# Performance work log

Measured on AMD Instinct MI355X. Metric: run time of the kernel, lower is better.

Reference implementation:

```python
import jax, jax.numpy as jnp
import numpy as np

B, T, D, E, H = 4, 1024, 1024, 8, 2048


def setup_inputs() -> dict:
    key = jax.random.key(0)
    ks = jax.random.split(key, 5)
    # Kaiming-uniform-ish init scales (exact values irrelevant for correctness baseline)
    bound_bank = 1.0 / np.sqrt(D)
    bound_down = 1.0 / np.sqrt(H)
    return {
        "x": jax.random.normal(ks[0], (B, T, D), dtype=jnp.float32),
        "gate_w": jax.random.uniform(ks[1], (E, D), jnp.float32, -bound_bank, bound_bank),
        "gate_bank": jax.random.uniform(ks[2], (E, D, H), jnp.float32, -bound_bank, bound_bank),
        "up_bank": jax.random.uniform(ks[3], (E, D, H), jnp.float32, -bound_bank, bound_bank),
        "down_bank": jax.random.uniform(ks[4], (E, H, D), jnp.float32, -bound_down, bound_down),
    }


def reference(x, gate_w, gate_bank, up_bank, down_bank):
    # Router logits: [B,T,E] (nn.Linear with weight [E,D], no bias)
    logits = jnp.einsum('btd,ed->bte', x, gate_w)
    selected = jnp.argmax(logits, axis=-1)          # [B,T] int
    # Dense all-expert SwiGLU
    u = jnp.einsum('btd,edh->bteh', x, up_bank)     # [B,T,E,H]
    a = jnp.einsum('btd,edh->bteh', x, gate_bank)   # [B,T,E,H]
    h = jax.nn.silu(a) * u                          # [B,T,E,H]
    y = jnp.einsum('bteh,ehd->bted', h, down_bank)  # [B,T,E,D]
    # Gather argmax-selected expert output per token
    idx = selected[:, :, None, None]                # [B,T,1,1]
    out = jnp.take_along_axis(y, idx, axis=2)[:, :, 0, :]  # [B,T,D]
    return out
```

## Files before the change

kernel.cpp:

```cpp
#include <hip/hip_runtime.h>
#include <hip/hip_bf16.h>

#define NTOK 4096
#define DDIM 1024
#define HDIM 2048
#define NEXP 8

typedef __attribute__((ext_vector_type(4))) float f32x4;
typedef __attribute__((ext_vector_type(8))) short bf16x8;
typedef __attribute__((ext_vector_type(8))) unsigned short us8;

__device__ __forceinline__ unsigned short f2bf(float f) {
    unsigned u = __float_as_uint(f);
    return (unsigned short)((u + 0x7fffu + ((u >> 16) & 1u)) >> 16);
}

__device__ __forceinline__ void gload16(const void* g, void* l) {
    __builtin_amdgcn_global_load_lds((const __attribute__((address_space(1))) void*)g,
                                     (__attribute__((address_space(3))) void*)l, 16, 0, 0);
}

__global__ void xcast(const float* __restrict__ x, unsigned short* __restrict__ xb) {
    int i = blockIdx.x * blockDim.x + threadIdx.x;
    float4 v = reinterpret_cast<const float4*>(x)[i];
    ushort4 o = { f2bf(v.x), f2bf(v.y), f2bf(v.z), f2bf(v.w) };
    reinterpret_cast<ushort4*>(xb)[i] = o;
}

__global__ __launch_bounds__(256) void tcast(const float* __restrict__ src,
        unsigned short* __restrict__ dst, int R, int C, int interleave, int upoff,
        long long estride) {
    __shared__ unsigned short __attribute__((aligned(16))) tile[64][80];
    const int e = blockIdx.z, r0 = blockIdx.y * 64, c0 = blockIdx.x * 64;
    const float* s = src + ((size_t)e * R + r0) * C + c0;
    const int t = threadIdx.x;
    const int rd = t >> 2;
    #pragma unroll
    for (int j = 0; j < 4; ++j) {
        int c4 = (t & 3) * 4 + j;
        float4 v = *reinterpret_cast<const float4*>(s + (size_t)rd * C + c4 * 4);
        tile[c4 * 4 + 0][rd] = f2bf(v.x);
        tile[c4 * 4 + 1][rd] = f2bf(v.y);
        tile[c4 * 4 + 2][rd] = f2bf(v.z);
        tile[c4 * 4 + 3][rd] = f2bf(v.w);
    }
    __syncthreads();
    const int cr = t >> 2;
    const int c = c0 + cr;
    const int orow = interleave ? (((c >> 4) << 5) + (c & 15) + upoff) : c;
    unsigned short* drow = dst + (size_t)e * estride + (size_t)orow * R + r0;
    #pragma unroll
    for (int j = 0; j < 2; ++j) {
        int ch = (t & 3) + j * 4;
        *reinterpret_cast<us8*>(drow + ch * 8) = *reinterpret_cast<const us8*>(&tile[cr][ch * 8]);
    }
}

__global__ void gate_kernel(const float* __restrict__ x, const float* __restrict__ gw,
                            int* __restrict__ sel) {
    int t = blockIdx.x;
    int tid = threadIdx.x, lane = tid & 63, w = tid >> 6;
    __shared__ double red[NEXP];
    const float* xr = x + (size_t)t * DDIM;
    #pragma unroll
    for (int s = 0; s < 2; ++s) {
        int e = w * 2 + s;
        const float* g = gw + (size_t)e * DDIM;
        double acc = 0.0;
        #pragma unroll
        for (int j = 0; j < DDIM / 64; ++j) {
            int d = lane + j * 64;
            acc += (double)xr[d] * (double)g[d];
        }
        #pragma unroll
        for (int off = 32; off; off >>= 1) acc += __shfl_down(acc, off);
        if (lane == 0) red[e] = acc;
    }
    __syncthreads();
    if (tid == 0) {
        int best = 0; double bv = red[0];
        #pragma unroll
        for (int e = 1; e < NEXP; ++e) if (red[e] > bv) { bv = red[e]; best = e; }
        sel[t] = best;
    }
}

__global__ void scatter_kernel(const int* __restrict__ sel, int* __restrict__ cnt,
                               int* __restrict__ perm) {
    int t = blockIdx.x * blockDim.x + threadIdx.x;
    if (t < NTOK) {
        int e = sel[t];
        int p = atomicAdd(&cnt[e], 1);
        perm[e * NTOK + p] = t;
    }
}

__global__ __launch_bounds__(256) void stage_a(
        const unsigned short* __restrict__ xb, const unsigned short* __restrict__ wa,
        const int* __restrict__ cnt, const int* __restrict__ perm,
        unsigned short* __restrict__ hws) {
    const int e = blockIdx.z;
    const int n0 = blockIdx.x * 128;
    const int m0 = blockIdx.y * 128;
    const int count = cnt[e];
    if (m0 >= count) return;
    const int* pl = perm + e * NTOK;

    __shared__ unsigned short __attribute__((aligned(16))) As[128 * 64];
    __shared__ unsigned short __attribute__((aligned(16))) Bs[128 * 64];

    const int tid = threadIdx.x, lane = tid & 63, w = tid >> 6;
    const int wr = w >> 1, wc = w & 1, li = lane & 15, lg = lane >> 4;
    const int sb = lane & 7, r8 = lane >> 3;
    const int srcswz = (sb ^ r8) * 8;

    const unsigned short* pA[4];
    const unsigned short* pB[4];
    #pragma unroll
    for (int i = 0; i < 4; ++i) {
        int row = i * 32 + w * 8 + r8;
        int tr = m0 + row; if (tr >= count) tr = count - 1;
        int tok = pl[tr];
        pA[i] = xb + (size_t)tok * DDIM + srcswz;
        pB[i] = wa + ((size_t)e * (2 * HDIM) + (size_t)(n0 + row)) * DDIM + srcswz;
    }

    f32x4 acc[4][4];
    #pragma unroll
    for (int i = 0; i < 4; ++i)
        #pragma unroll
        for (int j = 0; j < 4; ++j) acc[i][j] = (f32x4){0.f, 0.f, 0.f, 0.f};

    for (int k0 = 0; k0 < DDIM; k0 += 64) {
        #pragma unroll
        for (int i = 0; i < 4; ++i) gload16(pA[i] + k0, As + (i * 256 + w * 64) * 8);
        #pragma unroll
        for (int i = 0; i < 4; ++i) gload16(pB[i] + k0, Bs + (i * 256 + w * 64) * 8);
        asm volatile("s_waitcnt vmcnt(0)" ::: "memory");
        __syncthreads();
        #pragma unroll
        for (int kf = 0; kf < 2; ++kf) {
            bf16x8 a[4], b[4];
            const int kb = kf * 4 + lg;
            #pragma unroll
            for (int mi = 0; mi < 4; ++mi) {
                int r = wr * 64 + mi * 16 + li;
                a[mi] = *reinterpret_cast<const bf16x8*>(As + r * 64 + ((kb ^ (li & 7)) << 3));
            }
            #pragma unroll
            for (int ni = 0; ni < 4; ++ni) {
                int n = wc * 64 + ni * 16 + li;
                b[ni] = *reinterpret_cast<const bf16x8*>(Bs + n * 64 + ((kb ^ (li & 7)) << 3));
            }
            #pragma unroll
            for (int mi = 0; mi < 4; ++mi)
                #pragma unroll
                for (int ni = 0; ni < 4; ++ni)
                    acc[mi][ni] = __builtin_amdgcn_mfma_f32_16x16x32_bf16(a[mi], b[ni], acc[mi][ni], 0, 0, 0);
        }
        __syncthreads();
    }
    const int hbase = (n0 >> 1) + wc * 32 + li;
    #pragma unroll
    for (int mi = 0; mi < 4; ++mi) {
        #pragma unroll
        for (int r = 0; r < 4; ++r) {
            int row = m0 + wr * 64 + mi * 16 + lg * 4 + r;
            if (row < count) {
                int tok = pl[row];
                #pragma unroll
                for (int p = 0; p < 2; ++p) {
                    float a = acc[mi][p * 2 + 0][r];
                    float u = acc[mi][p * 2 + 1][r];
                    float h = (a / (1.f + __expf(-a))) * u;
                    hws[(size_t)tok * HDIM + hbase + p * 16] = f2bf(h);
                }
            }
        }
    }
}

__global__ __launch_bounds__(256) void stage_b(
        const unsigned short* __restrict__ hws, const unsigned short* __restrict__ wb,
        const int* __restrict__ cnt, const int* __restrict__ perm,
        float* __restrict__ out) {
    const int e = blockIdx.z;
    const int n0 = blockIdx.x * 128;
    const int m0 = blockIdx.y * 128;
    const int count = cnt[e];
    if (m0 >= count) return;
    const int* pl = perm + e * NTOK;

    __shared__ unsigned short __attribute__((aligned(16))) As[128 * 64];
    __shared__ unsigned short __attribute__((aligned(16))) Bs[128 * 64];

    const int tid = threadIdx.x, lane = tid & 63, w = tid >> 6;
    const int wr = w >> 1, wc = w & 1, li = lane & 15, lg = lane >> 4;
    const int sb = lane & 7, r8 = lane >> 3;
    const int srcswz = (sb ^ r8) * 8;

    const unsigned short* pA[4];
    const unsigned short* pB[4];
    #pragma unroll
    for (int i = 0; i < 4; ++i) {
        int row = i * 32 + w * 8 + r8;
        int tr = m0 + row; if (tr >= count) tr = count - 1;
        int tok = pl[tr];
        pA[i] = hws + (size_t)tok * HDIM + srcswz;
        pB[i] = wb + ((size_t)e * DDIM + (size_t)(n0 + row)) * HDIM + srcswz;
    }

    f32x4 acc[4][4];
    #pragma unroll
    for (int i = 0; i < 4; ++i)
        #pragma unroll
        for (int j = 0; j < 4; ++j) acc[i][j] = (f32x4){0.f, 0.f, 0.f, 0.f};

    for (int k0 = 0; k0 < HDIM; k0 += 64) {
        #pragma unroll
        for (int i = 0; i < 4; ++i) gload16(pA[i] + k0, As + (i * 256 + w * 64) * 8);
        #pragma unroll
        for (int i = 0; i < 4; ++i) gload16(pB[i] + k0, Bs + (i * 256 + w * 64) * 8);
        asm volatile("s_waitcnt vmcnt(0)" ::: "memory");
        __syncthreads();
        #pragma unroll
        for (int kf = 0; kf < 2; ++kf) {
            bf16x8 a[4], b[4];
            const int kb = kf * 4 + lg;
            #pragma unroll
            for (int mi = 0; mi < 4; ++mi) {
                int r = wr * 64 + mi * 16 + li;
                a[mi] = *reinterpret_cast<const bf16x8*>(As + r * 64 + ((kb ^ (li & 7)) << 3));
            }
            #pragma unroll
            for (int ni = 0; ni < 4; ++ni) {
                int n = wc * 64 + ni * 16 + li;
                b[ni] = *reinterpret_cast<const bf16x8*>(Bs + n * 64 + ((kb ^ (li & 7)) << 3));
            }
            #pragma unroll
            for (int mi = 0; mi < 4; ++mi)
                #pragma unroll
                for (int ni = 0; ni < 4; ++ni)
                    acc[mi][ni] = __builtin_amdgcn_mfma_f32_16x16x32_bf16(a[mi], b[ni], acc[mi][ni], 0, 0, 0);
        }
        __syncthreads();
    }
    #pragma unroll
    for (int mi = 0; mi < 4; ++mi) {
        #pragma unroll
        for (int r = 0; r < 4; ++r) {
            int row = m0 + wr * 64 + mi * 16 + lg * 4 + r;
            if (row < count) {
                int tok = pl[row];
                #pragma unroll
                for (int ni = 0; ni < 4; ++ni)
                    out[(size_t)tok * DDIM + n0 + wc * 64 + ni * 16 + li] = acc[mi][ni][r];
            }
        }
    }
}

extern "C" void kernel_launch(void* const* d_in, const int* in_sizes, int n_in,
                              void* d_out, int out_size, void* d_ws, size_t ws_size,
                              hipStream_t stream) {
    const float* x  = (const float*)d_in[0];
    const float* gw = (const float*)d_in[1];
    const float* gb = (const float*)d_in[2];
    const float* ub = (const float*)d_in[3];
    const float* db = (const float*)d_in[4];
    float* out = (float*)d_out;

    char* ws = (char*)d_ws;
    unsigned short* wbank = (unsigned short*)(ws);
    unsigned short* hws   = (unsigned short*)(ws + 67108864);
    unsigned short* xbf   = (unsigned short*)(ws + 67108864 + 16777216);
    char* misc = ws + 67108864 + 16777216 + 8388608;
    int* cnt  = (int*)(misc);
    int* sel  = (int*)(misc + 256);
    int* perm = (int*)(misc + 256 + 16384);

    hipMemsetAsync(cnt, 0, 256, stream);
    xcast<<<NTOK * DDIM / 4 / 256, 256, 0, stream>>>(x, xbf);
    tcast<<<dim3(HDIM / 64, DDIM / 64, NEXP), 256, 0, stream>>>(
        gb, wbank, DDIM, HDIM, 1, 0, (long long)2 * HDIM * DDIM);
    tcast<<<dim3(HDIM / 64, DDIM / 64, NEXP), 256, 0, stream>>>(
        ub, wbank, DDIM, HDIM, 1, 16, (long long)2 * HDIM * DDIM);
    gate_kernel<<<NTOK, 256, 0, stream>>>(x, gw, sel);
    scatter_kernel<<<NTOK / 256, 256, 0, stream>>>(sel, cnt, perm);
    stage_a<<<dim3(2 * HDIM / 128, NTOK / 128, NEXP), 256, 0, stream>>>(
        xbf, wbank, cnt, perm, hws);
    tcast<<<dim3(DDIM / 64, HDIM / 64, NEXP), 256, 0, stream>>>(
        db, wbank, HDIM, DDIM, 0, 0, (long long)DDIM * HDIM);
    stage_b<<<dim3(DDIM / 128, NTOK / 128, NEXP), 256, 0, stream>>>(
        hws, wbank, cnt, perm, out);
}
```

Baseline: 372.0 us.

## Double-buffer LDS in grouped GEMMs, fuse x cast with router, repad transpose tile

Both grouped GEMM stages now use two LDS buffers, so the global-to-LDS load for the next K tile is issued before the MFMAs on the current tile run, and one barrier per iteration is dropped. The bf16 cast of x and the router argmax are merged into a single per-token kernel that reads x once. The transpose-cast tile changes from 80-element rows read as 16-byte vectors to 65-element rows read element by element, aiming to cut LDS bank conflicts at the cost of scalar LDS reads. Doubling LDS to 64 KB per block may lower occupancy in the GEMM stages.

Measured after the change: 368.5 us. No clear change (-0.9%).

```diff
diff --git a/kernel.cpp b/kernel.cpp
--- a/kernel.cpp
+++ b/kernel.cpp
@@ -20,17 +20,54 @@
                                      (__attribute__((address_space(3))) void*)l, 16, 0, 0);
 }
 
-__global__ void xcast(const float* __restrict__ x, unsigned short* __restrict__ xb) {
-    int i = blockIdx.x * blockDim.x + threadIdx.x;
-    float4 v = reinterpret_cast<const float4*>(x)[i];
+__global__ __launch_bounds__(256) void xg_kernel(
+        const float* __restrict__ x, const float* __restrict__ gw,
+        unsigned short* __restrict__ xb, int* __restrict__ sel) {
+    const int t = blockIdx.x, tid = threadIdx.x, lane = tid & 63, w = tid >> 6;
+    const float4 v = *reinterpret_cast<const float4*>(x + (size_t)t * DDIM + tid * 4);
     ushort4 o = { f2bf(v.x), f2bf(v.y), f2bf(v.z), f2bf(v.w) };
-    reinterpret_cast<ushort4*>(xb)[i] = o;
+    *reinterpret_cast<ushort4*>(xb + (size_t)t * DDIM + tid * 4) = o;
+
+    double acc[NEXP];
+    #pragma unroll
+    for (int e = 0; e < NEXP; ++e) {
+        const float4 g = *reinterpret_cast<const float4*>(gw + (size_t)e * DDIM + tid * 4);
+        acc[e] = (double)v.x * g.x + (double)v.y * g.y + (double)v.z * g.z + (double)v.w * g.w;
+    }
+    __shared__ double red[4][NEXP];
+    #pragma unroll
+    for (int e = 0; e < NEXP; ++e) {
+        double a = acc[e];
+        #pragma unroll
+        for (int off = 32; off; off >>= 1) a += __shfl_down(a, off);
+        if (lane == 0) red[w][e] = a;
+    }
+    __syncthreads();
+    if (tid == 0) {
+        int best = 0; double bv = -1e300;
+        #pragma unroll
+        for (int e = 0; e < NEXP; ++e) {
+            double s = red[0][e] + red[1][e] + red[2][e] + red[3][e];
+            if (s > bv) { bv = s; best = e; }
+        }
+        sel[t] = best;
+    }
+}
+
+__global__ void scatter_kernel(const int* __restrict__ sel, int* __restrict__ cnt,
+                               int* __restrict__ perm) {
+    int t = blockIdx.x * blockDim.x + threadIdx.x;
+    if (t < NTOK) {
+        int e = sel[t];
+        int p = atomicAdd(&cnt[e], 1);
+        perm[e * NTOK + p] = t;
+    }
 }
 
 __global__ __launch_bounds__(256) void tcast(const float* __restrict__ src,
         unsigned short* __restrict__ dst, int R, int C, int interleave, int upoff,
         long long estride) {
-    __shared__ unsigned short __attribute__((aligned(16))) tile[64][80];
+    __shared__ unsigned short tile[64][65];
     const int e = blockIdx.z, r0 = blockIdx.y * 64, c0 = blockIdx.x * 64;
     const float* s = src + ((size_t)e * R + r0) * C + c0;
     const int t = threadIdx.x;
@@ -49,50 +86,14 @@
     const int c = c0 + cr;
     const int orow = interleave ? (((c >> 4) << 5) + (c & 15) + upoff) : c;
     unsigned short* drow = dst + (size_t)e * estride + (size_t)orow * R + r0;
-    #pragma unroll
-    for (int j = 0; j < 2; ++j) {
-        int ch = (t & 3) + j * 4;
-        *reinterpret_cast<us8*>(drow + ch * 8) = *reinterpret_cast<const us8*>(&tile[cr][ch * 8]);
-    }
-}
-
-__global__ void gate_kernel(const float* __restrict__ x, const float* __restrict__ gw,
-                            int* __restrict__ sel) {
-    int t = blockIdx.x;
-    int tid = threadIdx.x, lane = tid & 63, w = tid >> 6;
-    __shared__ double red[NEXP];
-    const float* xr = x + (size_t)t * DDIM;
-    #pragma unroll
-    for (int s = 0; s < 2; ++s) {
-        int e = w * 2 + s;
-        const float* g = gw + (size_t)e * DDIM;
-        double acc = 0.0;
-        #pragma unroll
-        for (int j = 0; j < DDIM / 64; ++j) {
-            int d = lane + j * 64;
-            acc += (double)xr[d] * (double)g[d];
-        }
-        #pragma unroll
-        for (int off = 32; off; off >>= 1) acc += __shfl_down(acc, off);
-        if (lane == 0) red[e] = acc;
-    }
-    __syncthreads();
-    if (tid == 0) {
-        int best = 0; double bv = red[0];
-        #pragma unroll
-        for (int e = 1; e < NEXP; ++e) if (red[e] > bv) { bv = red[e]; best = e; }
-        sel[t] = best;
-    }
-}
-
-__global__ void scatter_kernel(const int* __restrict__ sel, int* __restrict__ cnt,
-                               int* __restrict__ perm) {
-    int t = blockIdx.x * blockDim.x + threadIdx.x;
-    if (t < NTOK) {
-        int e = sel[t];
-        int p = atomicAdd(&cnt[e], 1);
-        perm[e * NTOK + p] = t;
-    }
+    const int rbase = (t & 3) * 16;
+    us8 v0, v1;
+    #pragma unroll
+    for (int s2 = 0; s2 < 8; ++s2) ((unsigned short*)&v0)[s2] = tile[cr][rbase + s2];
+    #pragma unroll
+    for (int s2 = 0; s2 < 8; ++s2) ((unsigned short*)&v1)[s2] = tile[cr][rbase + 8 + s2];
+    *reinterpret_cast<us8*>(drow + rbase) = v0;
+    *reinterpret_cast<us8*>(drow + rbase + 8) = v1;
 }
 
 __global__ __launch_bounds__(256) void stage_a(
@@ -106,8 +107,8 @@
     if (m0 >= count) return;
     const int* pl = perm + e * NTOK;
 
-    __shared__ unsigned short __attribute__((aligned(16))) As[128 * 64];
-    __shared__ unsigned short __attribute__((aligned(16))) Bs[128 * 64];
+    __shared__ unsigned short __attribute__((aligned(16))) As[2][128 * 64];
+    __shared__ unsigned short __attribute__((aligned(16))) Bs[2][128 * 64];
 
     const int tid = threadIdx.x, lane = tid & 63, w = tid >> 6;
     const int wr = w >> 1, wc = w & 1, li = lane & 15, lg = lane >> 4;
@@ -131,13 +132,23 @@
         #pragma unroll
         for (int j = 0; j < 4; ++j) acc[i][j] = (f32x4){0.f, 0.f, 0.f, 0.f};
 
-    for (int k0 = 0; k0 < DDIM; k0 += 64) {
-        #pragma unroll
-        for (int i = 0; i < 4; ++i) gload16(pA[i] + k0, As + (i * 256 + w * 64) * 8);
-        #pragma unroll
-        for (int i = 0; i < 4; ++i) gload16(pB[i] + k0, Bs + (i * 256 + w * 64) * 8);
-        asm volatile("s_waitcnt vmcnt(0)" ::: "memory");
-        __syncthreads();
+    #pragma unroll
+    for (int i = 0; i < 4; ++i) gload16(pA[i], &As[0][(i * 256 + w * 64) * 8]);
+    #pragma unroll
+    for (int i = 0; i < 4; ++i) gload16(pB[i], &Bs[0][(i * 256 + w * 64) * 8]);
+    asm volatile("s_waitcnt vmcnt(0)" ::: "memory");
+    __syncthreads();
+
+    int cur = 0;
+    const int NT = DDIM / 64;
+    for (int t = 0; t < NT; ++t) {
+        if (t + 1 < NT) {
+            const int k0 = (t + 1) * 64;
+            #pragma unroll
+            for (int i = 0; i < 4; ++i) gload16(pA[i] + k0, &As[cur ^ 1][(i * 256 + w * 64) * 8]);
+            #pragma unroll
+            for (int i = 0; i < 4; ++i) gload16(pB[i] + k0, &Bs[cur ^ 1][(i * 256 + w * 64) * 8]);
+        }
         #pragma unroll
         for (int kf = 0; kf < 2; ++kf) {
             bf16x8 a[4], b[4];
@@ -145,12 +156,12 @@
             #pragma unroll
             for (int mi = 0; mi < 4; ++mi) {
                 int r = wr * 64 + mi * 16 + li;
-                a[mi] = *reinterpret_cast<const bf16x8*>(As + r * 64 + ((kb ^ (li & 7)) << 3));
+                a[mi] = *reinterpret_cast<const bf16x8*>(&As[cur][r * 64 + ((kb ^ (li & 7)) << 3)]);
             }
             #pragma unroll
             for (int ni = 0; ni < 4; ++ni) {
                 int n = wc * 64 + ni * 16 + li;
-                b[ni] = *reinterpret_cast<const bf16x8*>(Bs + n * 64 + ((kb ^ (li & 7)) << 3));
+                b[ni] = *reinterpret_cast<const bf16x8*>(&Bs[cur][n * 64 + ((kb ^ (li & 7)) << 3)]);
             }
             #pragma unroll
             for (int mi = 0; mi < 4; ++mi)
@@ -158,7 +169,11 @@
                 for (int ni = 0; ni < 4; ++ni)
                     acc[mi][ni] = __builtin_amdgcn_mfma_f32_16x16x32_bf16(a[mi], b[ni], acc[mi][ni], 0, 0, 0);
         }
-        __syncthreads();
+        if (t + 1 < NT) {
+            asm volatile("s_waitcnt vmcnt(0)" ::: "memory");
+            __syncthreads();
+            cur ^= 1;
+        }
     }
     const int hbase = (n0 >> 1) + wc * 32 + li;
     #pragma unroll
@@ -191,8 +206,8 @@
     if (m0 >= count) return;
     const int* pl = perm + e * NTOK;
 
-    __shared__ unsigned short __attribute__((aligned(16))) As[128 * 64];
-    __shared__ unsigned short __attribute__((aligned(16))) Bs[128 * 64];
+    __shared__ unsigned short __attribute__((aligned(16))) As[2][128 * 64];
+    __shared__ unsigned short __attribute__((aligned(16))) Bs[2][128 * 64];
 
     const int tid = threadIdx.x, lane = tid & 63, w = tid >> 6;
     const int wr = w >> 1, wc = w & 1, li = lane & 15, lg = lane >> 4;
@@ -216,13 +231,23 @@
         #pragma unroll
         for (int j = 0; j < 4; ++j) acc[i][j] = (f32x4){0.f, 0.f, 0.f, 0.f};
 
-    for (int k0 = 0; k0 < HDIM; k0 += 64) {
-        #pragma unroll
-        for (int i = 0; i < 4; ++i) gload16(pA[i] + k0, As + (i * 256 + w * 64) * 8);
-        #pragma unroll
-        for (int i = 0; i < 4; ++i) gload16(pB[i] + k0, Bs + (i * 256 + w * 64) * 8);
-        asm volatile("s_waitcnt vmcnt(0)" ::: "memory");
-        __syncthreads();
+    #pragma unroll
+    for (int i = 0; i < 4; ++i) gload16(pA[i], &As[0][(i * 256 + w * 64) * 8]);
+    #pragma unroll
+    for (int i = 0; i < 4; ++i) gload16(pB[i], &Bs[0][(i * 256 + w * 64) * 8]);
+    asm volatile("s_waitcnt vmcnt(0)" ::: "memory");
+    __syncthreads();
+
+    int cur = 0;
+    const int NT = HDIM / 64;
+    for (int t = 0; t < NT; ++t) {
+        if (t + 1 < NT) {
+            const int k0 = (t + 1) * 64;
+            #pragma unroll
+            for (int i = 0; i < 4; ++i) gload16(pA[i] + k0, &As[cur ^ 1][(i * 256 + w * 64) * 8]);
+            #pragma unroll
+            for (int i = 0; i < 4; ++i) gload16(pB[i] + k0, &Bs[cur ^ 1][(i * 256 + w * 64) * 8]);
+        }
         #pragma unroll
         for (int kf = 0; kf < 2; ++kf) {
             bf16x8 a[4], b[4];
@@ -230,12 +255,12 @@
             #pragma unroll
             for (int mi = 0; mi < 4; ++mi) {
                 int r = wr * 64 + mi * 16 + li;
-                a[mi] = *reinterpret_cast<const bf16x8*>(As + r * 64 + ((kb ^ (li & 7)) << 3));
+                a[mi] = *reinterpret_cast<const bf16x8*>(&As[cur][r * 64 + ((kb ^ (li & 7)) << 3)]);
             }
             #pragma unroll
             for (int ni = 0; ni < 4; ++ni) {
                 int n = wc * 64 + ni * 16 + li;
-                b[ni] = *reinterpret_cast<const bf16x8*>(Bs + n * 64 + ((kb ^ (li & 7)) << 3));
+                b[ni] = *reinterpret_cast<const bf16x8*>(&Bs[cur][n * 64 + ((kb ^ (li & 7)) << 3)]);
             }
             #pragma unroll
             for (int mi = 0; mi < 4; ++mi)
@@ -243,7 +268,11 @@
                 for (int ni = 0; ni < 4; ++ni)
                     acc[mi][ni] = __builtin_amdgcn_mfma_f32_16x16x32_bf16(a[mi], b[ni], acc[mi][ni], 0, 0, 0);
         }
-        __syncthreads();
+        if (t + 1 < NT) {
+            asm volatile("s_waitcnt vmcnt(0)" ::: "memory");
+            __syncthreads();
+            cur ^= 1;
+        }
     }
     #pragma unroll
     for (int mi = 0; mi < 4; ++mi) {
@@ -280,12 +309,11 @@
     int* perm = (int*)(misc + 256 + 16384);
 
     hipMemsetAsync(cnt, 0, 256, stream);
-    xcast<<<NTOK * DDIM / 4 / 256, 256, 0, stream>>>(x, xbf);
+    xg_kernel<<<NTOK, 256, 0, stream>>>(x, gw, xbf, sel);
     tcast<<<dim3(HDIM / 64, DDIM / 64, NEXP), 256, 0, stream>>>(
         gb, wbank, DDIM, HDIM, 1, 0, (long long)2 * HDIM * DDIM);
     tcast<<<dim3(HDIM / 64, DDIM / 64, NEXP), 256, 0, stream>>>(
         ub, wbank, DDIM, HDIM, 1, 16, (long long)2 * HDIM * DDIM);
-    gate_kernel<<<NTOK, 256, 0, stream>>>(x, gw, sel);
     scatter_kernel<<<NTOK / 256, 256, 0, stream>>>(sel, cnt, perm);
     stage_a<<<dim3(2 * HDIM / 128, NTOK / 128, NEXP), 256, 0, stream>>>(
         xbf, wbank, cnt, perm, hws);
```
